# Kernel tuning notes

Measured on AMD Instinct MI355X. Metric: run time of the kernel, lower is better.

## Reference

```python
import jax, jax.numpy as jnp
import numpy as np

V, J, NB = 6890, 52, 16
NPOSE = (J - 1) * 9  # 459 pose-blendshape features
# Standard SMPL-H kinematic tree: 22 body joints + left hand (wrist 20) + right hand (wrist 21)
PARENTS = np.array([
    -1, 0, 0, 0, 1, 2, 3, 4, 5, 6, 7, 8, 9, 9, 9, 12, 13, 14, 16, 17, 18, 19,
    20, 22, 23, 20, 25, 26, 20, 28, 29, 20, 31, 32, 20, 34, 35,
    21, 37, 38, 21, 40, 41, 21, 43, 44, 21, 46, 47, 21, 49, 50
], dtype=np.int32)


def rot6d_to_matrix(d6):
    # d6: (..., 6) -> (..., 3, 3), rows are the Gram-Schmidt basis (pytorch3d convention)
    a1, a2 = d6[..., :3], d6[..., 3:]
    b1 = a1 / jnp.linalg.norm(a1, axis=-1, keepdims=True)
    a2p = a2 - jnp.sum(b1 * a2, axis=-1, keepdims=True) * b1
    b2 = a2p / jnp.linalg.norm(a2p, axis=-1, keepdims=True)
    b3 = jnp.cross(b1, b2)
    return jnp.stack([b1, b2, b3], axis=-2)


def rigid_transform(rot_mats, joints):
    # rot_mats: (B, J, 3, 3); joints: (B, J, 3) -> relative transforms (B, J, 4, 4)
    rel = jnp.concatenate(
        [joints[..., :1, :], joints[..., 1:, :] - joints[..., PARENTS[1:], :]], axis=-2)
    tm = jnp.concatenate([rot_mats, rel[..., None]], axis=-1)  # (B, J, 3, 4)
    bottom = jnp.zeros(tm.shape[:-2] + (1, 4), dtype=tm.dtype).at[..., 0, 3].set(1.0)
    tm = jnp.concatenate([tm, bottom], axis=-2)  # (B, J, 4, 4)
    chain = [tm[..., 0, :, :]]
    for i in range(1, J):  # fixed 52-joint tree, unrolled
        chain.append(chain[int(PARENTS[i])] @ tm[..., i, :, :])
    transforms = jnp.stack(chain, axis=-3)  # (B, J, 4, 4)
    t_corr = jnp.einsum('bjcd,bjd->bjc', transforms[..., :3, :3], joints)
    return transforms.at[..., :3, 3].add(-t_corr)


def lbs_forward(body_pose, betas, global_orient, transl,
                v_template, shapedirs, posedirs, J_template, J_shapedirs, lbs_weights):
    full_pose = jnp.concatenate([global_orient, body_pose], axis=-2)  # (B, 52, 6)
    rot_mats = rot6d_to_matrix(full_pose)                              # (B, 52, 3, 3)
    joints = J_template + jnp.einsum('bk,jck->bjc', betas, J_shapedirs)
    A = rigid_transform(rot_mats, joints)                              # (B, 52, 4, 4)
    eye = jnp.eye(3, dtype=rot_mats.dtype)
    pose_feature = (rot_mats[..., 1:, :, :] - eye).reshape(rot_mats.shape[0], NPOSE)
    v_posed = (v_template
               + jnp.einsum('bk,vck->bvc', betas, shapedirs)
               + jnp.einsum('bk,kvc->bvc', pose_feature, posedirs))    # (B, V, 3)
    T = jnp.einsum('vj,bjcd->bvcd', lbs_weights, A)                    # (B, V, 4, 4)
    verts = jnp.einsum('bvcd,bvd->bvc', T[..., :3, :3], v_posed) + T[..., :3, 3]
    return verts + transl[..., None, :]


def setup_inputs() -> dict:
    key = jax.random.key(0)
    ks = jax.random.split(key, 10)
    B = 1024
    return {
        'body_pose': jax.random.normal(ks[0], (B, J - 1, 6), jnp.float32),
        'betas': jax.random.normal(ks[1], (B, NB), jnp.float32),
        'global_orient': jax.random.normal(ks[2], (B, 1, 6), jnp.float32),
        'transl': jax.random.normal(ks[3], (B, 3), jnp.float32),
        'v_template': jax.random.normal(ks[4], (V, 3), jnp.float32) * 0.3,
        'shapedirs': jax.random.normal(ks[5], (V, 3, NB), jnp.float32) * 0.01,
        'posedirs': jax.random.normal(ks[6], (NPOSE, V, 3), jnp.float32) * 0.01,
        'J_template': jax.random.normal(ks[7], (J, 3), jnp.float32) * 0.3,
        'J_shapedirs': jax.random.normal(ks[8], (J, 3, NB), jnp.float32) * 0.01,
        'lbs_weights': jax.nn.softmax(jax.random.normal(ks[9], (V, J), jnp.float32) * 2.0, axis=-1),
    }


def reference(body_pose, betas, global_orient, transl,
              v_template, shapedirs, posedirs, J_template, J_shapedirs, lbs_weights):
    return lbs_forward(body_pose, betas, global_orient, transl,
                       v_template, shapedirs, posedirs, J_template, J_shapedirs, lbs_weights)
```

## Files before the change

### kernel.cpp

```cpp
#include <hip/hip_runtime.h>

typedef unsigned short u16;
typedef __bf16  bf16x8 __attribute__((ext_vector_type(8)));
typedef float   f32x4  __attribute__((ext_vector_type(4)));
typedef unsigned int u32x4 __attribute__((ext_vector_type(4)));

#define B_SZ   1024
#define V_SZ   6890
#define VPADB  6912
#define J_SZ   52
#define NB_SZ  16
#define NPOSE  459
#define N3     20670
#define NPAD   20736
#define KG     480
#define KA     160
#define MROWS  12288

#define NK1    (B_SZ / 4)
#define NK0W   (VPADB / 64)
#define NK0    (648 * 15)

__constant__ int PARENTS_D[52] = {-1,0,0,0,1,2,3,4,5,6,7,8,9,9,9,12,13,14,16,17,18,19,20,22,23,
                                  20,25,26,20,28,29,20,31,32,20,34,35,21,37,38,21,40,41,21,43,44,
                                  21,46,47,21,49,50};

__device__ __forceinline__ u16 f2b(float f) {
  union { float f; unsigned u; } v; v.f = f;
  unsigned r = (v.u + 0x7FFFu + ((v.u >> 16) & 1u)) >> 16;
  return (u16)r;
}
__device__ __forceinline__ float b2f(u16 h) {
  union { unsigned u; float f; } v; v.u = ((unsigned)h) << 16;
  return v.f;
}
__device__ __forceinline__ void async16(const void* g, void* l) {
  __builtin_amdgcn_global_load_lds((const __attribute__((address_space(1))) void*)g,
                                   (__attribute__((address_space(3))) void*)l, 16, 0, 0);
}

__global__ __launch_bounds__(256) void k_prep(const float* __restrict__ posedirs,
                                              const float* __restrict__ shapedirs,
                                              const float* __restrict__ lbsw,
                                              const float* __restrict__ body_pose,
                                              const float* __restrict__ betas,
                                              const float* __restrict__ global_orient,
                                              const float* __restrict__ J_template,
                                              const float* __restrict__ J_shapedirs,
                                              u16* __restrict__ PDt,
                                              u16* __restrict__ WB,
                                              u16* __restrict__ AH,
                                              u16* __restrict__ PF)
{
  __shared__ __align__(16) char smem[35328];
  const int bid = blockIdx.x;
  const int tid = threadIdx.x;

  if (bid < NK1) {
    const int g = tid >> 6;
    const int t = tid & 63;
    const int b = bid * 4 + g;
    char* base = smem + g * 8832;
    float (*R)[9]   = (float(*)[9])(base);
    float (*jts)[3] = (float(*)[3])(base + 1872);
    float (*G)[12]  = (float(*)[12])(base + 2496);
    u16*   AHs      = (u16*)(base + 4992);

    for (int i = t; i < 12 * KA / 2; i += 64) ((unsigned*)AHs)[i] = 0u;

    if (t < J_SZ) {
      const float* d6 = (t == 0) ? &global_orient[(size_t)b * 6]
                                 : &body_pose[((size_t)b * 51 + (t - 1)) * 6];
      float a1x = d6[0], a1y = d6[1], a1z = d6[2];
      float a2x = d6[3], a2y = d6[4], a2z = d6[5];
      float inv1 = rsqrtf(a1x*a1x + a1y*a1y + a1z*a1z);
      float b1x = a1x*inv1, b1y = a1y*inv1, b1z = a1z*inv1;
      float d   = b1x*a2x + b1y*a2y + b1z*a2z;
      float ux = a2x - d*b1x, uy = a2y - d*b1y, uz = a2z - d*b1z;
      float inv2 = rsqrtf(ux*ux + uy*uy + uz*uz);
      float b2x = ux*inv2, b2y = uy*inv2, b2z = uz*inv2;
      float b3x = b1y*b2z - b1z*b2y;
      float b3y = b1z*b2x - b1x*b2z;
      float b3z = b1x*b2y - b1y*b2x;
      R[t][0]=b1x; R[t][1]=b1y; R[t][2]=b1z;
      R[t][3]=b2x; R[t][4]=b2y; R[t][5]=b2z;
      R[t][6]=b3x; R[t][7]=b3y; R[t][8]=b3z;
#pragma unroll
      for (int c = 0; c < 3; ++c) {
        float s = J_template[t*3 + c];
#pragma unroll
        for (int k = 0; k < NB_SZ; ++k)
          s += betas[(size_t)b*NB_SZ + k] * J_shapedirs[(t*3 + c)*NB_SZ + k];
        jts[t][c] = s;
      }
    }
    __syncthreads();

    if (t < 3) {
      const int c = t;
      G[0][c*4+0] = R[0][c*3+0];
      G[0][c*4+1] = R[0][c*3+1];
      G[0][c*4+2] = R[0][c*3+2];
      G[0][c*4+3] = jts[0][c];
      for (int j = 1; j < J_SZ; ++j) {
        int p = PARENTS_D[j];
        float r0 = jts[j][0] - jts[p][0];
        float r1 = jts[j][1] - jts[p][1];
        float r2 = jts[j][2] - jts[p][2];
        float g0 = G[p][c*4+0], g1 = G[p][c*4+1], g2 = G[p][c*4+2];
        G[j][c*4+0] = g0*R[j][0] + g1*R[j][3] + g2*R[j][6];
        G[j][c*4+1] = g0*R[j][1] + g1*R[j][4] + g2*R[j][7];
        G[j][c*4+2] = g0*R[j][2] + g1*R[j][5] + g2*R[j][8];
        G[j][c*4+3] = g0*r0 + g1*r1 + g2*r2 + G[p][c*4+3];
      }
    }
    __syncthreads();

    if (t < J_SZ) {
      float o[12];
#pragma unroll
      for (int i = 0; i < 12; ++i) o[i] = G[t][i];
#pragma unroll
      for (int c = 0; c < 3; ++c)
        o[c*4+3] -= o[c*4+0]*jts[t][0] + o[c*4+1]*jts[t][1] + o[c*4+2]*jts[t][2];
#pragma unroll
      for (int cd = 0; cd < 12; ++cd) {
        u16 hi = f2b(o[cd]);
        u16 lo = f2b(o[cd] - b2f(hi));
        AHs[cd*KA + t]        = hi;
        AHs[cd*KA + 52 + t]   = lo;
        AHs[cd*KA + 104 + t]  = hi;
      }
    }

    for (int k = t; k < KG; k += 64) {
      float val = 0.f;
      if (k < NPOSE) {
        int j  = k / 9 + 1;
        int rc = k - (j - 1) * 9;
        val = R[j][rc] - ((rc == 0 || rc == 4 || rc == 8) ? 1.f : 0.f);
      } else if (k < NPOSE + NB_SZ) {
        val = betas[(size_t)b*NB_SZ + (k - NPOSE)];
      }
      PF[(size_t)b*KG + k] = f2b(val);
    }

    __syncthreads();
    unsigned* dst = (unsigned*)(AH + (size_t)b * 12 * KA);
    for (int i = t; i < 12 * KA / 2; i += 64) dst[i] = ((const unsigned*)AHs)[i];

  } else if (bid < NK1 + NK0W) {
    u16* wtile = (u16*)smem;
    const int v0  = (bid - NK1) * 64;
    const int vl  = tid >> 2;
    const int v   = v0 + vl;
    const int jseg = (tid & 3) * 13;

    wtile[vl * KA + 156 + (tid & 3)] = 0;

#pragma unroll
    for (int jj = 0; jj < 13; ++jj) {
      int j = jseg + jj;
      float wv = (v < V_SZ) ? lbsw[(size_t)v * J_SZ + j] : 0.f;
      u16 hi = f2b(wv);
      u16 lo = f2b(wv - b2f(hi));
      wtile[vl * KA + j]        = hi;
      wtile[vl * KA + 52 + j]   = hi;
      wtile[vl * KA + 104 + j]  = lo;
    }
    __syncthreads();
    u32x4*       dst = (u32x4*)(WB + (size_t)v0 * KA);
    const u32x4* src = (const u32x4*)wtile;
    for (int i = tid; i < 64 * KA / 8; i += 256) dst[i] = src[i];

  } else {
    u16 (*tile)[33] = (u16(*)[33])smem;
    const int cb = bid - NK1 - NK0W;
    const int tx = tid & 31;
    const int ty = tid >> 5;
    const int n0 = (cb % 648) * 32;
    const int k0 = (cb / 648) * 32;
#pragma unroll
    for (int i = 0; i < 4; ++i) {
      int k = k0 + ty + i*8;
      int n = n0 + tx;
      float val = 0.f;
      if (n < N3) {
        if (k < NPOSE)              val = posedirs[(size_t)k * N3 + n];
        else if (k < NPOSE + NB_SZ) val = shapedirs[(size_t)n * NB_SZ + (k - NPOSE)];
      }
      tile[ty + i*8][tx] = f2b(val);
    }
    __syncthreads();
#pragma unroll
    for (int i = 0; i < 4; ++i) {
      int n = n0 + ty + i*8;
      int k = k0 + tx;
      PDt[(size_t)n * KG + k] = tile[tx][ty + i*8];
    }
  }
}

__global__ __launch_bounds__(256) void k2_gemm(const u16* __restrict__ PF,
                                               const u16* __restrict__ PDt,
                                               const float* __restrict__ vtmpl,
                                               u16* __restrict__ VP)
{
  __shared__ __align__(16) u16 lA[2][4096];
  __shared__ __align__(16) u16 lB[2][4096];
  const int tid  = threadIdx.x;
  const int lane = tid & 63;
  const int w    = tid >> 6;
  const int n0   = blockIdx.x * 128;
  const int b0   = blockIdx.y * 128;
  const int moff = (w & 1) * 64;
  const int noff = (w >> 1) * 64;
  const int q    = lane >> 4;
  const int lrow = lane & 15;

  f32x4 acc[4][4];
#pragma unroll
  for (int i = 0; i < 4; ++i)
#pragma unroll
    for (int j = 0; j < 4; ++j) { f32x4 z = {0.f,0.f,0.f,0.f}; acc[i][j] = z; }

  int aoff[4], boff[4];
#pragma unroll
  for (int i = 0; i < 4; ++i) {
    int ra = moff + i*16 + lrow;
    aoff[i] = ra*32 + (q ^ ((ra + (ra >> 2)) & 3)) * 8;
    int rb = noff + i*16 + lrow;
    boff[i] = rb*32 + (q ^ ((rb + (rb >> 2)) & 3)) * 8;
  }
  int srow[2], schunk[2];
#pragma unroll
  for (int t = 0; t < 2; ++t) {
    int i = (t*4 + w)*64 + lane;
    int r = i >> 2;
    srow[t]   = r;
    schunk[t] = (i & 3) ^ ((r + (r >> 2)) & 3);
  }

#define K2_STAGE(buf, seg)                                                          \
  {                                                                                 \
    const int kk = (seg) * 32;                                                      \
    _Pragma("unroll")                                                               \
    for (int t = 0; t < 2; ++t) {                                                   \
      async16(PF  + (size_t)(b0 + srow[t])*KG + kk + schunk[t]*8,                   \
              &lA[buf][(t*4 + w)*512]);                                             \
      async16(PDt + (size_t)(n0 + srow[t])*KG + kk + schunk[t]*8,                   \
              &lB[buf][(t*4 + w)*512]);                                             \
    }                                                                               \
  }

  K2_STAGE(0, 0);
  __syncthreads();

  for (int seg = 0; seg < 15; ++seg) {
    const int cur = seg & 1;
    if (seg < 14) K2_STAGE(cur ^ 1, seg + 1);
    bf16x8 af[4], bfv[4];
#pragma unroll
    for (int i = 0; i < 4; ++i) af[i]  = *(const bf16x8*)&lA[cur][aoff[i]];
#pragma unroll
    for (int i = 0; i < 4; ++i) bfv[i] = *(const bf16x8*)&lB[cur][boff[i]];
#pragma unroll
    for (int i = 0; i < 4; ++i)
#pragma unroll
      for (int j = 0; j < 4; ++j)
        acc[i][j] = __builtin_amdgcn_mfma_f32_16x16x32_bf16(af[i], bfv[j], acc[i][j], 0, 0, 0);
    if (seg < 14) __syncthreads();
  }
#undef K2_STAGE

#pragma unroll
  for (int i = 0; i < 4; ++i) {
    int brow = b0 + moff + i*16 + q*4;
#pragma unroll
    for (int j = 0; j < 4; ++j) {
      int n = n0 + noff + j*16 + lrow;
      if (n < N3) {
        float bias = vtmpl[n];
#pragma unroll
        for (int r = 0; r < 4; ++r)
          VP[(size_t)(brow + r)*NPAD + n] = f2b(acc[i][j][r] + bias);
      }
    }
  }
}

__global__ __launch_bounds__(256) void k4_blend(const u16* __restrict__ AH,
                                                const u16* __restrict__ WB,
                                                const u16* __restrict__ VP,
                                                const float* __restrict__ transl,
                                                float* __restrict__ out)
{
  __shared__ __align__(16) u16 lA[2][4096];
  __shared__ __align__(16) u16 lB[2][4096];
  const int tid  = threadIdx.x;
  const int lane = tid & 63;
  const int w    = tid >> 6;
  const int n0   = blockIdx.x * 128;
  const int m0   = blockIdx.y * 128;
  const int moff = (w & 1) * 64;
  const int noff = (w >> 1) * 64;
  const int q    = lane >> 4;
  const int lrow = lane & 15;

  int srow[2], schunk[2];
#pragma unroll
  for (int t = 0; t < 2; ++t) {
    int i = (t*4 + w)*64 + lane;
    int r = i >> 2;
    srow[t]   = r;
    schunk[t] = (i & 3) ^ ((r + (r >> 2)) & 3);
  }

#define K4_STAGE(buf, seg)                                                          \
  {                                                                                 \
    const int kk = (seg) * 32;                                                      \
    _Pragma("unroll")                                                               \
    for (int t = 0; t < 2; ++t) {                                                   \
      async16(AH + (size_t)(m0 + srow[t])*KA + kk + schunk[t]*8,                    \
              &lA[buf][(t*4 + w)*512]);                                             \
      async16(WB + (size_t)(n0 + srow[t])*KA + kk + schunk[t]*8,                    \
              &lB[buf][(t*4 + w)*512]);                                             \
    }                                                                               \
  }

  K4_STAGE(0, 0);

  int   bp[4], cp[4];
  float tr[4];
#pragma unroll
  for (int i = 0; i < 4; ++i) {
    int gq = (m0 + moff + i*16) / 4 + q;
    bp[i] = gq / 3;
    cp[i] = gq - bp[i]*3;
    tr[i] = transl[bp[i]*3 + cp[i]];
  }
  u16 pv[4][4][3];
#pragma unroll
  for (int i = 0; i < 4; ++i) {
    const u16* vpb = VP + (size_t)bp[i] * NPAD;
#pragma unroll
    for (int j = 0; j < 4; ++j) {
      const int v = n0 + noff + j*16 + lrow;
      pv[i][j][0] = vpb[(size_t)v*3 + 0];
      pv[i][j][1] = vpb[(size_t)v*3 + 1];
      pv[i][j][2] = vpb[(size_t)v*3 + 2];
    }
  }

  f32x4 acc[4][4];
#pragma unroll
  for (int i = 0; i < 4; ++i)
#pragma unroll
    for (int j = 0; j < 4; ++j) { f32x4 z = {0.f,0.f,0.f,0.f}; acc[i][j] = z; }

  int aoff[4], boff[4];
#pragma unroll
  for (int i = 0; i < 4; ++i) {
    int ra = moff + i*16 + lrow;
    aoff[i] = ra*32 + (q ^ ((ra + (ra >> 2)) & 3)) * 8;
    int rb = noff + i*16 + lrow;
    boff[i] = rb*32 + (q ^ ((rb + (rb >> 2)) & 3)) * 8;
  }

  __syncthreads();

#pragma unroll
  for (int seg = 0; seg < 5; ++seg) {
    const int cur = seg & 1;
    if (seg < 4) K4_STAGE(cur ^ 1, seg + 1);
    bf16x8 af[4], bfv[4];
#pragma unroll
    for (int i = 0; i < 4; ++i) af[i]  = *(const bf16x8*)&lA[cur][aoff[i]];
#pragma unroll
    for (int i = 0; i < 4; ++i) bfv[i] = *(const bf16x8*)&lB[cur][boff[i]];
#pragma unroll
    for (int i = 0; i < 4; ++i)
#pragma unroll
      for (int j = 0; j < 4; ++j)
        acc[i][j] = __builtin_amdgcn_mfma_f32_16x16x32_bf16(af[i], bfv[j], acc[i][j], 0, 0, 0);
    if (seg < 4) __syncthreads();
  }
#undef K4_STAGE

#pragma unroll
  for (int i = 0; i < 4; ++i) {
    float* ob = out + (size_t)bp[i] * (V_SZ * 3);
#pragma unroll
    for (int j = 0; j < 4; ++j) {
      const int v = n0 + noff + j*16 + lrow;
      if (v < V_SZ) {
        float p0 = b2f(pv[i][j][0]);
        float p1 = b2f(pv[i][j][1]);
        float p2 = b2f(pv[i][j][2]);
        f32x4 a = acc[i][j];
        ob[(size_t)v*3 + cp[i]] = a[0]*p0 + a[1]*p1 + a[2]*p2 + a[3] + tr[i];
      }
    }
  }
}

extern "C" void kernel_launch(void* const* d_in, const int* in_sizes, int n_in,
                              void* d_out, int out_size, void* d_ws, size_t ws_size,
                              hipStream_t stream) {
  const float* body_pose     = (const float*)d_in[0];
  const float* betas         = (const float*)d_in[1];
  const float* global_orient = (const float*)d_in[2];
  const float* transl        = (const float*)d_in[3];
  const float* v_template    = (const float*)d_in[4];
  const float* shapedirs     = (const float*)d_in[5];
  const float* posedirs      = (const float*)d_in[6];
  const float* J_template    = (const float*)d_in[7];
  const float* J_shapedirs   = (const float*)d_in[8];
  const float* lbsw          = (const float*)d_in[9];
  float* out = (float*)d_out;

  char* ws = (char*)d_ws;
  u16* PF  = (u16*)(ws);
  u16* AH  = (u16*)(ws + 1048576u);
  u16* WB  = (u16*)(ws + 6291456u);
  u16* PDt = (u16*)(ws + 8503296u);
  u16* VP  = (u16*)(ws + 28409856u);

  k_prep<<<dim3(NK1 + NK0W + NK0), dim3(256), 0, stream>>>(
      posedirs, shapedirs, lbsw, body_pose, betas, global_orient,
      J_template, J_shapedirs, PDt, WB, AH, PF);
  k2_gemm<<<dim3(162, 8), dim3(256), 0, stream>>>(PF, PDt, v_template, VP);
  k4_blend<<<dim3(VPADB / 128, MROWS / 128), dim3(256), 0, stream>>>(AH, WB, VP, transl, out);
}
```

Baseline: 269.1 us.

## Use component-major posed-vertex layout and overlap async loads with MFMA via vmcnt waits

Posedirs are now laid out component-major (c, v) in the transposed weight buffer, so the posed-vertex output VP is stored as three contiguous planes of VPADB. The blend kernel can then read each component with coalesced per-vertex loads instead of stride-3 loads. Both GEMM loops replace __syncthreads with explicit s_waitcnt vmcnt(4) plus s_barrier, so the next stage's async copies stay in flight while the current stage computes. The blend kernel also issues its VP and transl loads before the first async stage so the vmcnt counting stays consistent. The risk is that the hand-counted vmcnt values are fragile if the compiler reorders or adds memory operations.

```diff
diff --git a/kernel.cpp b/kernel.cpp
--- a/kernel.cpp
+++ b/kernel.cpp
@@ -196,7 +196,9 @@
     for (int i = 0; i < 4; ++i) {
       int n = n0 + ty + i*8;
       int k = k0 + tx;
-      PDt[(size_t)n * KG + k] = tile[tx][ty + i*8];
+      int vv = n / 3;
+      int cc = n - vv * 3;
+      PDt[((size_t)cc * VPADB + vv) * KG + k] = tile[tx][ty + i*8];
     }
   }
 }
@@ -254,11 +256,15 @@
   }
 
   K2_STAGE(0, 0);
-  __syncthreads();
 
   for (int seg = 0; seg < 15; ++seg) {
     const int cur = seg & 1;
     if (seg < 14) K2_STAGE(cur ^ 1, seg + 1);
+    __builtin_amdgcn_sched_barrier(0);
+    if (seg < 14) asm volatile("s_waitcnt vmcnt(4)" ::: "memory");
+    else          asm volatile("s_waitcnt vmcnt(0)" ::: "memory");
+    __builtin_amdgcn_s_barrier();
+    __builtin_amdgcn_sched_barrier(0);
     bf16x8 af[4], bfv[4];
 #pragma unroll
     for (int i = 0; i < 4; ++i) af[i]  = *(const bf16x8*)&lA[cur][aoff[i]];
@@ -269,7 +275,10 @@
 #pragma unroll
       for (int j = 0; j < 4; ++j)
         acc[i][j] = __builtin_amdgcn_mfma_f32_16x16x32_bf16(af[i], bfv[j], acc[i][j], 0, 0, 0);
-    if (seg < 14) __syncthreads();
+    if (seg < 14) {
+      __builtin_amdgcn_sched_barrier(0);
+      __builtin_amdgcn_s_barrier();
+    }
   }
 #undef K2_STAGE
 
@@ -278,13 +287,13 @@
     int brow = b0 + moff + i*16 + q*4;
 #pragma unroll
     for (int j = 0; j < 4; ++j) {
-      int n = n0 + noff + j*16 + lrow;
-      if (n < N3) {
-        float bias = vtmpl[n];
-#pragma unroll
-        for (int r = 0; r < 4; ++r)
-          VP[(size_t)(brow + r)*NPAD + n] = f2b(acc[i][j][r] + bias);
-      }
+      int np = n0 + noff + j*16 + lrow;
+      int vv = np % VPADB;
+      int cc = np / VPADB;
+      float bias = (vv < V_SZ) ? vtmpl[vv*3 + cc] : 0.f;
+#pragma unroll
+      for (int r = 0; r < 4; ++r)
+        VP[(size_t)(brow + r)*NPAD + np] = f2b(acc[i][j][r] + bias);
     }
   }
 }
@@ -328,16 +337,12 @@
     }                                                                               \
   }
 
-  K4_STAGE(0, 0);
-
   int   bp[4], cp[4];
-  float tr[4];
 #pragma unroll
   for (int i = 0; i < 4; ++i) {
     int gq = (m0 + moff + i*16) / 4 + q;
     bp[i] = gq / 3;
     cp[i] = gq - bp[i]*3;
-    tr[i] = transl[bp[i]*3 + cp[i]];
   }
   u16 pv[4][4][3];
 #pragma unroll
@@ -346,11 +351,16 @@
 #pragma unroll
     for (int j = 0; j < 4; ++j) {
       const int v = n0 + noff + j*16 + lrow;
-      pv[i][j][0] = vpb[(size_t)v*3 + 0];
-      pv[i][j][1] = vpb[(size_t)v*3 + 1];
-      pv[i][j][2] = vpb[(size_t)v*3 + 2];
-    }
-  }
+      pv[i][j][0] = vpb[0*VPADB + v];
+      pv[i][j][1] = vpb[1*VPADB + v];
+      pv[i][j][2] = vpb[2*VPADB + v];
+    }
+  }
+  float tr[4];
+#pragma unroll
+  for (int i = 0; i < 4; ++i) tr[i] = transl[bp[i]*3 + cp[i]];
+
+  K4_STAGE(0, 0);
 
   f32x4 acc[4][4];
 #pragma unroll
@@ -367,12 +377,15 @@
     boff[i] = rb*32 + (q ^ ((rb + (rb >> 2)) & 3)) * 8;
   }
 
-  __syncthreads();
-
 #pragma unroll
   for (int seg = 0; seg < 5; ++seg) {
     const int cur = seg & 1;
     if (seg < 4) K4_STAGE(cur ^ 1, seg + 1);
+    __builtin_amdgcn_sched_barrier(0);
+    if (seg < 4) asm volatile("s_waitcnt vmcnt(4)" ::: "memory");
+    else         asm volatile("s_waitcnt vmcnt(0)" ::: "memory");
+    __builtin_amdgcn_s_barrier();
+    __builtin_amdgcn_sched_barrier(0);
     bf16x8 af[4], bfv[4];
 #pragma unroll
     for (int i = 0; i < 4; ++i) af[i]  = *(const bf16x8*)&lA[cur][aoff[i]];
@@ -383,7 +396,10 @@
 #pragma unroll
       for (int j = 0; j < 4; ++j)
         acc[i][j] = __builtin_amdgcn_mfma_f32_16x16x32_bf16(af[i], bfv[j], acc[i][j], 0, 0, 0);
-    if (seg < 4) __syncthreads();
+    if (seg < 4) {
+      __builtin_amdgcn_sched_barrier(0);
+      __builtin_amdgcn_s_barrier();
+    }
   }
 #undef K4_STAGE
 
```

After: 253.0 us. -6.0%, faster.
